# Performance work log

Measured on AMD Instinct MI355X. Metric: run time of the kernel, lower is better.

The kernel has to match this reference:

```python
import jax, jax.numpy as jnp
import numpy as np

D = 1024
H = 16
HD = D // H
FF = 4 * D
EPS = 1e-5


def _layernorm(x, scale, shift):
    # Faithful to the torch module: unbiased std (ddof=1), eps added to std.
    mean = jnp.mean(x, axis=-1, keepdims=True)
    var = jnp.sum((x - mean) ** 2, axis=-1, keepdims=True) / (x.shape[-1] - 1)
    std = jnp.sqrt(var)
    return shift + scale * (x - mean) / (std + EPS)


def _gelu(x):
    c = jnp.sqrt(jnp.asarray(2.0 / jnp.pi, dtype=x.dtype))
    return 0.5 * x * (1.0 + jnp.tanh(c * (x + 0.044715 * x ** 3)))


def setup_inputs() -> dict:
    key = jax.random.key(0)
    ks = jax.random.split(key, 8)
    B, S = 2, 2048
    inv = 1.0 / np.sqrt(D)
    x = jax.random.normal(ks[0], (B, S, D), dtype=jnp.float32)
    scale1 = jnp.ones((D,), jnp.float32)
    shift1 = jnp.zeros((D,), jnp.float32)
    Wqkv = jax.random.normal(ks[1], (3 * D, D), jnp.float32) * inv  # torch layout [out,in]
    Wo_w = jax.random.normal(ks[2], (D, D), jnp.float32) * inv
    Wo_b = jnp.zeros((D,), jnp.float32)
    scale2 = jnp.ones((D,), jnp.float32)
    shift2 = jnp.zeros((D,), jnp.float32)
    W1 = jax.random.normal(ks[3], (FF, D), jnp.float32) * inv
    b1 = jnp.zeros((FF,), jnp.float32)
    W2 = jax.random.normal(ks[4], (D, FF), jnp.float32) * (1.0 / np.sqrt(FF))
    b2 = jnp.zeros((D,), jnp.float32)
    return {"x": x, "scale1": scale1, "shift1": shift1, "Wqkv": Wqkv,
            "Wo_w": Wo_w, "Wo_b": Wo_b, "scale2": scale2, "shift2": shift2,
            "W1": W1, "b1": b1, "W2": W2, "b2": b2}


def reference(x, scale1, shift1, Wqkv, Wo_w, Wo_b, scale2, shift2, W1, b1, W2, b2):
    B, S, _ = x.shape
    # --- pre-norm attention ---
    h = _layernorm(x, scale1, shift1)
    qkv = jnp.einsum('bsd,ed->bse', h, Wqkv)  # [B,S,3D]
    q, k, v = jnp.split(qkv, 3, axis=-1)
    q = q.reshape(B, S, H, HD).transpose(0, 2, 1, 3)  # [B,H,S,HD]
    k = k.reshape(B, S, H, HD).transpose(0, 2, 1, 3)
    v = v.reshape(B, S, H, HD).transpose(0, 2, 1, 3)
    scores = jnp.einsum('bhqd,bhkd->bhqk', q, k) / jnp.sqrt(jnp.asarray(HD, x.dtype))
    causal = jnp.triu(jnp.ones((S, S), dtype=bool), k=1)
    scores = jnp.where(causal, -jnp.inf, scores)
    weights = jax.nn.softmax(scores, axis=-1)
    attn = jnp.einsum('bhqk,bhkd->bhqd', weights, v)
    attn = attn.transpose(0, 2, 1, 3).reshape(B, S, D)
    attn = jnp.einsum('bsd,ed->bse', attn, Wo_w) + Wo_b
    x = x + attn
    # --- pre-norm MLP ---
    h2 = _layernorm(x, scale2, shift2)
    m = _gelu(jnp.einsum('bsd,fd->bsf', h2, W1) + b1)
    m = jnp.einsum('bsf,df->bsd', m, W2) + b2
    return x + m
```

## Files before the change

kernel.cpp:

```cpp
#include <hip/hip_runtime.h>
#include <cstdint>
#include <cstddef>

typedef __bf16 bf16;
typedef __bf16 v8bf __attribute__((ext_vector_type(8)));
typedef __bf16 v4bf __attribute__((ext_vector_type(4)));
typedef float  v4f  __attribute__((ext_vector_type(4)));

#define D_MODEL 1024
#define FF_DIM  4096
#define SEQ     2048
#define NTOK    4096
#define NH      16
#define HDIM    64

#define GLOAD_LDS16(g, l) \
    __builtin_amdgcn_global_load_lds((const __attribute__((address_space(1))) void*)(g), \
                                     (__attribute__((address_space(3))) void*)(l), 16, 0, 0)

__global__ __launch_bounds__(256) void prep_kernel(
    const float* __restrict__ Wqkv, const float* __restrict__ Wo,
    const float* __restrict__ W1, const float* __restrict__ W2,
    bf16* __restrict__ Wqkv_b, bf16* __restrict__ Wo_b,
    bf16* __restrict__ W1_b, bf16* __restrict__ W2_b) {
    int u = blockIdx.x * 256 + threadIdx.x;
    const float* src; bf16* dst; int idx;
    if (u < 786432)       { src = Wqkv; dst = Wqkv_b; idx = u * 4; }
    else if (u < 1048576) { src = Wo;   dst = Wo_b;   idx = (u - 786432) * 4; }
    else if (u < 2097152) { src = W1;   dst = W1_b;   idx = (u - 1048576) * 4; }
    else                  { src = W2;   dst = W2_b;   idx = (u - 2097152) * 4; }
    float4 v = *(const float4*)(src + idx);
    dst[idx + 0] = (bf16)v.x;
    dst[idx + 1] = (bf16)v.y;
    dst[idx + 2] = (bf16)v.z;
    dst[idx + 3] = (bf16)v.w;
}

__global__ __launch_bounds__(256) void layernorm_kernel(
    const float* __restrict__ x, const float* __restrict__ scale,
    const float* __restrict__ shift, bf16* __restrict__ out) {
    int row = blockIdx.x;
    int t = threadIdx.x;
    const float* xr = x + (size_t)row * D_MODEL;
    float4 v = *(const float4*)(xr + t * 4);
    float s  = v.x + v.y + v.z + v.w;
    float sq = v.x * v.x + v.y * v.y + v.z * v.z + v.w * v.w;
    #pragma unroll
    for (int o = 1; o < 64; o <<= 1) {
        s  += __shfl_xor(s, o);
        sq += __shfl_xor(sq, o);
    }
    __shared__ float ws[8];
    int wv = t >> 6;
    if ((t & 63) == 0) { ws[wv * 2] = s; ws[wv * 2 + 1] = sq; }
    __syncthreads();
    s  = ws[0] + ws[2] + ws[4] + ws[6];
    sq = ws[1] + ws[3] + ws[5] + ws[7];
    float mean = s * (1.0f / D_MODEL);
    float var  = (sq - (float)D_MODEL * mean * mean) * (1.0f / (D_MODEL - 1));
    var = fmaxf(var, 0.0f);
    float inv = 1.0f / (sqrtf(var) + 1e-5f);
    #pragma unroll
    for (int j = 0; j < 4; ++j) {
        int c = t * 4 + j;
        float xv = (&v.x)[j];
        out[(size_t)row * D_MODEL + c] = (bf16)(shift[c] + scale[c] * (xv - mean) * inv);
    }
}

__global__ __launch_bounds__(256) void transpose_v(
    const bf16* __restrict__ vb, bf16* __restrict__ vt) {
    int bh = blockIdx.x >> 5;
    int ts = blockIdx.x & 31;
    int t = threadIdx.x;
    __shared__ bf16 T[64][72];
    const bf16* src = vb + ((size_t)bh * SEQ + ts * 64) * HDIM;
    #pragma unroll
    for (int half = 0; half < 2; ++half) {
        int s = (t >> 3) + half * 32;
        int d0 = (t & 7) * 8;
        v8bf vv = *(const v8bf*)(src + (size_t)s * HDIM + d0);
        #pragma unroll
        for (int j = 0; j < 8; ++j) T[d0 + j][s] = vv[j];
    }
    __syncthreads();
    bf16* dst = vt + (size_t)bh * HDIM * SEQ + ts * 64;
    int d = t >> 2;
    #pragma unroll
    for (int cc = 0; cc < 2; ++cc) {
        int c = (t & 3) + cc * 4;
        v8bf o = *(const v8bf*)(&T[d][c * 8]);
        *(v8bf*)(dst + (size_t)d * SEQ + c * 8) = o;
    }
}

template <int EPI>
__global__ __launch_bounds__(256) void gemm_nt(
    const bf16* __restrict__ A, const bf16* __restrict__ Bw,
    const float* __restrict__ bias, const float* __restrict__ resid,
    float* __restrict__ outf, bf16* __restrict__ ob0,
    bf16* __restrict__ ob1, bf16* __restrict__ ob2,
    int M, int N, int K, int klen) {
    __shared__ __align__(16) bf16 As[128 * 64];
    __shared__ __align__(16) bf16 Bs[128 * 64];
    int m0 = blockIdx.y * 128, n0 = blockIdx.x * 128;
    int kstart = blockIdx.z * klen;
    int t = threadIdx.x;
    int lane = t & 63, wave = t >> 6;
    int wm = wave >> 1, wn = wave & 1;
    int quad = lane >> 4, l16 = lane & 15;

    int srow8 = lane >> 3;
    int schunk = (lane & 7) ^ srow8;
    const bf16* agp = A  + (size_t)(m0 + wave * 8 + srow8) * K + kstart + schunk * 8;
    const bf16* bgp = Bw + (size_t)(n0 + wave * 8 + srow8) * K + kstart + schunk * 8;
    size_t row32 = (size_t)32 * K;

    v4f acc[4][4];
    #pragma unroll
    for (int i = 0; i < 4; ++i)
        #pragma unroll
        for (int j = 0; j < 4; ++j)
            acc[i][j] = (v4f){0.f, 0.f, 0.f, 0.f};

    int rsw = l16 & 7;
    for (int kk = 0; kk < klen; kk += 64) {
        __syncthreads();
        #pragma unroll
        for (int ii = 0; ii < 4; ++ii) {
            GLOAD_LDS16(agp + ii * row32 + kk, &As[ii * 2048 + wave * 512]);
            GLOAD_LDS16(bgp + ii * row32 + kk, &Bs[ii * 2048 + wave * 512]);
        }
        __syncthreads();
        #pragma unroll
        for (int h = 0; h < 2; ++h) {
            v8bf af[4], bfr[4];
            #pragma unroll
            for (int i = 0; i < 4; ++i)
                af[i] = *(const v8bf*)(&As[(wm * 64 + i * 16 + l16) * 64 + (((h * 4 + quad) ^ rsw)) * 8]);
            #pragma unroll
            for (int j = 0; j < 4; ++j)
                bfr[j] = *(const v8bf*)(&Bs[(wn * 64 + j * 16 + l16) * 64 + (((h * 4 + quad) ^ rsw)) * 8]);
            #pragma unroll
            for (int i = 0; i < 4; ++i)
                #pragma unroll
                for (int j = 0; j < 4; ++j)
                    acc[i][j] = __builtin_amdgcn_mfma_f32_16x16x32_bf16(af[i], bfr[j], acc[i][j], 0, 0, 0);
        }
    }

    #pragma unroll
    for (int i = 0; i < 4; ++i) {
        #pragma unroll
        for (int j = 0; j < 4; ++j) {
            #pragma unroll
            for (int r = 0; r < 4; ++r) {
                float v = acc[i][j][r];
                int row = m0 + wm * 64 + i * 16 + quad * 4 + r;
                int col = n0 + wn * 64 + j * 16 + l16;
                if (EPI == 0) {
                    int which = col >> 10, rr = col & 1023;
                    int h = rr >> 6, d = rr & 63;
                    int b = row >> 11, sI = row & 2047;
                    size_t dst = (((size_t)(b * NH + h)) * SEQ + sI) * HDIM + d;
                    if (which == 0)      ob0[dst] = (bf16)(v * 0.125f);
                    else if (which == 1) ob1[dst] = (bf16)v;
                    else                 ob2[dst] = (bf16)v;
                } else if (EPI == 1) {
                    size_t o = (size_t)row * N + col;
                    outf[o] = resid[o] + v + bias[col];
                } else if (EPI == 2) {
                    float u = v + bias[col];
                    float y = 1.5957691216057308f * (u + 0.044715f * u * u * u);
                    float g = u * __builtin_amdgcn_rcpf(1.0f + __expf(-y));
                    ob0[(size_t)row * N + col] = (bf16)g;
                } else {
                    ob0[(size_t)blockIdx.z * M * N + (size_t)row * N + col] = (bf16)v;
                }
            }
        }
    }
}

__global__ __launch_bounds__(256) void combine_w2(
    const bf16* __restrict__ part, const float* __restrict__ x1,
    const float* __restrict__ b2, float* __restrict__ out) {
    int i = (blockIdx.x * 256 + threadIdx.x) * 4;
    int col = i & (D_MODEL - 1);
    float4 xv = *(const float4*)(x1 + i);
    float4 bv = *(const float4*)(b2 + col);
    float4 r;
    r.x = xv.x + bv.x; r.y = xv.y + bv.y; r.z = xv.z + bv.z; r.w = xv.w + bv.w;
    #pragma unroll
    for (int z = 0; z < 4; ++z) {
        v4bf p = *(const v4bf*)(part + (size_t)z * NTOK * D_MODEL + i);
        r.x += (float)p[0]; r.y += (float)p[1]; r.z += (float)p[2]; r.w += (float)p[3];
    }
    *(float4*)(out + i) = r;
}

__global__ __launch_bounds__(256) void attn_kernel(
    const bf16* __restrict__ qb, const bf16* __restrict__ kb,
    const bf16* __restrict__ vt, float* __restrict__ pO0,
    float* __restrict__ pO1, float* __restrict__ L0,
    float* __restrict__ L1) {
    int u = (int)gridDim.x - 1 - (int)blockIdx.x;
    int bh = u / 48;
    int r48 = u - bh * 48;
    int qt, st;
    if (r48 < 16) { qt = r48; st = 0; }
    else          { qt = 16 + ((r48 - 16) >> 1); st = (r48 - 16) & 1; }
    int qbase = qt * 64;
    int kv0 = st * 1024;
    int kv1 = min(qbase + 64, kv0 + 1024);
    float* pO = st ? pO1 : pO0;
    float* L  = st ? L1 : L0;

    int t = threadIdx.x;
    int wave = t >> 6, lane = t & 63;
    int quad = lane >> 4, l16 = lane & 15;
    int qwb = qbase + wave * 16;

    const bf16* Qh  = qb + (size_t)bh * SEQ * HDIM;
    const bf16* Kh  = kb + (size_t)bh * SEQ * HDIM;
    const bf16* Vth = vt + (size_t)bh * HDIM * SEQ;

    __shared__ __align__(16) bf16 Ks[64 * 64];
    __shared__ __align__(16) bf16 Vs[64 * 64];
    __shared__ __align__(16) bf16 Ps[4][16 * 80];
    bf16* Pw = &Ps[wave][0];

    int u0 = t, u1 = t + 256;
    int key0 = u0 >> 3, c0 = (u0 & 7) ^ (key0 & 7);
    int key1 = u1 >> 3, c1 = (u1 & 7) ^ (key1 & 7);
    bf16* kdst0 = &Ks[wave * 512];
    bf16* kdst1 = &Ks[2048 + wave * 512];
    bf16* vdst0 = &Vs[wave * 512];
    bf16* vdst1 = &Vs[2048 + wave * 512];
    const bf16* Ksrc0 = Kh + (size_t)key0 * HDIM + c0 * 8;
    const bf16* Ksrc1 = Kh + (size_t)key1 * HDIM + c1 * 8;
    const bf16* Vsrc0 = Vth + (size_t)key0 * SEQ + c0 * 8;
    const bf16* Vsrc1 = Vth + (size_t)key1 * SEQ + c1 * 8;

    v8bf qf0 = *(const v8bf*)(Qh + (size_t)(qwb + l16) * HDIM + quad * 8);
    v8bf qf1 = *(const v8bf*)(Qh + (size_t)(qwb + l16) * HDIM + 32 + quad * 8);

    v4f o[4];
    #pragma unroll
    for (int dc = 0; dc < 4; ++dc) o[dc] = (v4f){0.f, 0.f, 0.f, 0.f};
    float lsum = 0.f;

    for (int kv = kv0; kv < kv1; kv += 64) {
        __syncthreads();
        GLOAD_LDS16(Ksrc0 + (size_t)kv * HDIM, kdst0);
        GLOAD_LDS16(Ksrc1 + (size_t)kv * HDIM, kdst1);
        GLOAD_LDS16(Vsrc0 + kv, vdst0);
        GLOAD_LDS16(Vsrc1 + kv, vdst1);
        __syncthreads();

        bool domask = (kv + 63 > qwb);
        #pragma unroll
        for (int j = 0; j < 4; ++j) {
            int key = j * 16 + l16;
            v8bf ka = *(const v8bf*)(&Ks[(key * 8 + (quad ^ (key & 7))) * 8]);
            v8bf kc = *(const v8bf*)(&Ks[(key * 8 + ((quad + 4) ^ (key & 7))) * 8]);
            v4f s = (v4f){-20.f, -20.f, -20.f, -20.f};
            s = __builtin_amdgcn_mfma_f32_16x16x32_bf16(ka, qf0, s, 0, 0, 0);
            s = __builtin_amdgcn_mfma_f32_16x16x32_bf16(kc, qf1, s, 0, 0, 0);
            int keyb = kv + j * 16 + quad * 4;
            union { bf16 h[4]; uint2 u; } pk;
            #pragma unroll
            for (int r = 0; r < 4; ++r) {
                float pv = __expf(s[r]);
                if (domask) pv = (keyb + r <= qwb + l16) ? pv : 0.f;
                lsum += pv;
                pk.h[r] = (bf16)pv;
            }
            *(uint2*)(&Pw[l16 * 80 + j * 16 + quad * 4]) = pk.u;
        }

        v8bf pf0 = *(const v8bf*)(&Pw[l16 * 80 + quad * 8]);
        v8bf pf1 = *(const v8bf*)(&Pw[l16 * 80 + 32 + quad * 8]);
        #pragma unroll
        for (int dc = 0; dc < 4; ++dc) {
            int dim = dc * 16 + l16;
            v8bf va = *(const v8bf*)(&Vs[(dim * 8 + (quad ^ (dim & 7))) * 8]);
            v8bf vc = *(const v8bf*)(&Vs[(dim * 8 + ((quad + 4) ^ (dim & 7))) * 8]);
            o[dc] = __builtin_amdgcn_mfma_f32_16x16x32_bf16(pf0, va, o[dc], 0, 0, 0);
            o[dc] = __builtin_amdgcn_mfma_f32_16x16x32_bf16(pf1, vc, o[dc], 0, 0, 0);
        }
    }

    lsum += __shfl_xor(lsum, 16);
    lsum += __shfl_xor(lsum, 32);
    if (quad == 0) L[(size_t)bh * SEQ + qwb + l16] = lsum;

    #pragma unroll
    for (int r = 0; r < 4; ++r) {
        int row = qwb + quad * 4 + r;
        #pragma unroll
        for (int dc = 0; dc < 4; ++dc) {
            pO[((size_t)bh * SEQ + row) * HDIM + dc * 16 + l16] = o[dc][r];
        }
    }
}

__global__ __launch_bounds__(256) void attn_finalize(
    const float* __restrict__ pO0, const float* __restrict__ pO1,
    const float* __restrict__ L0, const float* __restrict__ L1,
    bf16* __restrict__ ob) {
    int i = (blockIdx.x * 256 + threadIdx.x) * 4;
    int bh = i >> 17;
    int rem = i & 131071;
    int s = rem >> 6, d0 = rem & 63;
    float l = L0[(size_t)bh * SEQ + s];
    float4 o = *(const float4*)(pO0 + i);
    if ((s >> 6) >= 16) {
        l += L1[(size_t)bh * SEQ + s];
        float4 o1 = *(const float4*)(pO1 + i);
        o.x += o1.x; o.y += o1.y; o.z += o1.z; o.w += o1.w;
    }
    float inv = 1.0f / l;
    int b = bh >> 4, h = bh & 15;
    bf16* dst = ob + ((size_t)(b * SEQ + s)) * D_MODEL + h * HDIM + d0;
    dst[0] = (bf16)(o.x * inv);
    dst[1] = (bf16)(o.y * inv);
    dst[2] = (bf16)(o.z * inv);
    dst[3] = (bf16)(o.w * inv);
}

extern "C" void kernel_launch(void* const* d_in, const int* in_sizes, int n_in,
                              void* d_out, int out_size, void* d_ws, size_t ws_size,
                              hipStream_t stream) {
    const float* x      = (const float*)d_in[0];
    const float* scale1 = (const float*)d_in[1];
    const float* shift1 = (const float*)d_in[2];
    const float* Wqkv   = (const float*)d_in[3];
    const float* Wo_w   = (const float*)d_in[4];
    const float* Wo_b   = (const float*)d_in[5];
    const float* scale2 = (const float*)d_in[6];
    const float* shift2 = (const float*)d_in[7];
    const float* W1     = (const float*)d_in[8];
    const float* b1     = (const float*)d_in[9];
    const float* W2     = (const float*)d_in[10];
    const float* b2     = (const float*)d_in[11];
    float* out = (float*)d_out;

    char* ws = (char*)d_ws;
    size_t off = 0;
    auto alloc = [&](size_t bytes) -> char* {
        char* p = ws + off;
        off += (bytes + 255) & ~(size_t)255;
        return p;
    };
    bf16* Wqkv_b = (bf16*)alloc((size_t)3 * D_MODEL * D_MODEL * 2);
    bf16* Wo_bf  = (bf16*)alloc((size_t)D_MODEL * D_MODEL * 2);
    bf16* W1_b   = (bf16*)alloc((size_t)FF_DIM * D_MODEL * 2);
    bf16* W2_b   = (bf16*)alloc((size_t)D_MODEL * FF_DIM * 2);
    bf16* bufA   = (bf16*)alloc((size_t)NTOK * D_MODEL * 2);
    bf16* qb     = (bf16*)alloc((size_t)NTOK * D_MODEL * 2);
    bf16* kb     = (bf16*)alloc((size_t)NTOK * D_MODEL * 2);
    bf16* vb     = (bf16*)alloc((size_t)NTOK * D_MODEL * 2);
    bf16* vtb    = (bf16*)alloc((size_t)NTOK * D_MODEL * 2);
    float* x1    = (float*)alloc((size_t)NTOK * D_MODEL * 4);
    bf16* mbuf   = (bf16*)alloc((size_t)NTOK * FF_DIM * 2);
    float* pO0 = (float*)mbuf;
    float* L0  = pO0 + (size_t)32 * SEQ * HDIM;
    float* L1  = L0 + (size_t)32 * SEQ;
    float* pO1 = x1;
    bf16* w2part = bufA;
    (void)ws_size; (void)n_in; (void)in_sizes; (void)out_size;

    prep_kernel<<<12288, 256, 0, stream>>>(Wqkv, Wo_w, W1, W2,
                                           Wqkv_b, Wo_bf, W1_b, W2_b);

    layernorm_kernel<<<NTOK, 256, 0, stream>>>(x, scale1, shift1, bufA);

    gemm_nt<0><<<dim3(3072 / 128, NTOK / 128), 256, 0, stream>>>(
        bufA, Wqkv_b, nullptr, nullptr, nullptr, qb, kb, vb, NTOK, 3072, D_MODEL, D_MODEL);

    transpose_v<<<1024, 256, 0, stream>>>(vb, vtb);

    attn_kernel<<<1536, 256, 0, stream>>>(qb, kb, vtb, pO0, pO1, L0, L1);
    attn_finalize<<<32 * SEQ * HDIM / 1024, 256, 0, stream>>>(pO0, pO1, L0, L1, bufA);

    gemm_nt<1><<<dim3(D_MODEL / 128, NTOK / 128), 256, 0, stream>>>(
        bufA, Wo_bf, Wo_b, x, x1, nullptr, nullptr, nullptr, NTOK, D_MODEL, D_MODEL, D_MODEL);

    layernorm_kernel<<<NTOK, 256, 0, stream>>>(x1, scale2, shift2, qb);

    gemm_nt<2><<<dim3(FF_DIM / 128, NTOK / 128), 256, 0, stream>>>(
        qb, W1_b, b1, nullptr, nullptr, mbuf, nullptr, nullptr, NTOK, FF_DIM, D_MODEL, D_MODEL);

    gemm_nt<6><<<dim3(D_MODEL / 128, NTOK / 128, 4), 256, 0, stream>>>(
        mbuf, W2_b, nullptr, nullptr, nullptr, w2part, nullptr, nullptr, NTOK, D_MODEL, FF_DIM, FF_DIM / 4);

    combine_w2<<<NTOK * D_MODEL / 1024, 256, 0, stream>>>(w2part, x1, b2, out);
}
```

Before: 361.4 us.

## Pair causal query tiles per block, skip masked subtiles, fuse attention finalize

Attention now gives each block two query tiles (tile i and tile 31-i) so every block has the same causal workload, and K/V tiles loaded once are shared between the two tiles. Work past the diagonal is skipped at 16/32-key granularity. Normalisation moves into the kernel epilogue, which removes the split-KV partial buffers and the separate finalize launch. Softmax switches to exp2 by folding log2e into the Q scale and the fixed max shift. The grid shrinks to 512 blocks of 256 threads, so occupancy may fall, and each block must keep two sets of accumulators in registers.

```diff
diff --git a/kernel.cpp b/kernel.cpp
--- a/kernel.cpp
+++ b/kernel.cpp
@@ -17,6 +17,9 @@
 #define GLOAD_LDS16(g, l) \
     __builtin_amdgcn_global_load_lds((const __attribute__((address_space(1))) void*)(g), \
                                      (__attribute__((address_space(3))) void*)(l), 16, 0, 0)
+
+#define QSCALE 0.18033688011112042f
+#define SHIFT2 -28.853900817779268f
 
 __global__ __launch_bounds__(256) void prep_kernel(
     const float* __restrict__ Wqkv, const float* __restrict__ Wo,
@@ -163,7 +166,7 @@
                     int h = rr >> 6, d = rr & 63;
                     int b = row >> 11, sI = row & 2047;
                     size_t dst = (((size_t)(b * NH + h)) * SEQ + sI) * HDIM + d;
-                    if (which == 0)      ob0[dst] = (bf16)(v * 0.125f);
+                    if (which == 0)      ob0[dst] = (bf16)(v * QSCALE);
                     else if (which == 1) ob1[dst] = (bf16)v;
                     else                 ob2[dst] = (bf16)v;
                 } else if (EPI == 1) {
@@ -199,27 +202,62 @@
     *(float4*)(out + i) = r;
 }
 
+__device__ __forceinline__ void attn_process_tile(
+    int kv, int qwb, int quad, int l16,
+    const bf16* Ks, const bf16* Vs, bf16* Pw,
+    const v8bf& qf0, const v8bf& qf1, v4f (&o)[4], float& lsum) {
+    #pragma unroll
+    for (int hh = 0; hh < 2; ++hh) {
+        int kb32 = kv + hh * 32;
+        if (kb32 > qwb + 15) break;
+        #pragma unroll
+        for (int j2 = 0; j2 < 2; ++j2) {
+            int j = hh * 2 + j2;
+            int kb16 = kb32 + j2 * 16;
+            union { bf16 h[4]; uint2 u; } pk;
+            if (kb16 > qwb + 15) {
+                pk.u = (uint2){0u, 0u};
+            } else {
+                int key = j * 16 + l16;
+                v8bf ka = *(const v8bf*)(&Ks[(key * 8 + (quad ^ (key & 7))) * 8]);
+                v8bf kc = *(const v8bf*)(&Ks[(key * 8 + ((quad + 4) ^ (key & 7))) * 8]);
+                v4f s = (v4f){SHIFT2, SHIFT2, SHIFT2, SHIFT2};
+                s = __builtin_amdgcn_mfma_f32_16x16x32_bf16(ka, qf0, s, 0, 0, 0);
+                s = __builtin_amdgcn_mfma_f32_16x16x32_bf16(kc, qf1, s, 0, 0, 0);
+                bool dm = (kb16 + 15 > qwb);
+                int keyb = kb16 + quad * 4;
+                #pragma unroll
+                for (int r = 0; r < 4; ++r) {
+                    float pv = __builtin_amdgcn_exp2f(s[r]);
+                    if (dm) pv = (keyb + r <= qwb + l16) ? pv : 0.f;
+                    lsum += pv;
+                    pk.h[r] = (bf16)pv;
+                }
+            }
+            *(uint2*)(&Pw[l16 * 80 + j * 16 + quad * 4]) = pk.u;
+        }
+        v8bf pf = *(const v8bf*)(&Pw[l16 * 80 + hh * 32 + quad * 8]);
+        #pragma unroll
+        for (int dc = 0; dc < 4; ++dc) {
+            int dim = dc * 16 + l16;
+            v8bf vv = *(const v8bf*)(&Vs[(dim * 8 + ((quad + 4 * hh) ^ (dim & 7))) * 8]);
+            o[dc] = __builtin_amdgcn_mfma_f32_16x16x32_bf16(pf, vv, o[dc], 0, 0, 0);
+        }
+    }
+}
+
 __global__ __launch_bounds__(256) void attn_kernel(
     const bf16* __restrict__ qb, const bf16* __restrict__ kb,
-    const bf16* __restrict__ vt, float* __restrict__ pO0,
-    float* __restrict__ pO1, float* __restrict__ L0,
-    float* __restrict__ L1) {
-    int u = (int)gridDim.x - 1 - (int)blockIdx.x;
-    int bh = u / 48;
-    int r48 = u - bh * 48;
-    int qt, st;
-    if (r48 < 16) { qt = r48; st = 0; }
-    else          { qt = 16 + ((r48 - 16) >> 1); st = (r48 - 16) & 1; }
-    int qbase = qt * 64;
-    int kv0 = st * 1024;
-    int kv1 = min(qbase + 64, kv0 + 1024);
-    float* pO = st ? pO1 : pO0;
-    float* L  = st ? L1 : L0;
+    const bf16* __restrict__ vt, bf16* __restrict__ ob) {
+    int bh = blockIdx.x >> 4;
+    int pr = blockIdx.x & 15;
+    int qtA = pr, qtB = 31 - pr;
 
     int t = threadIdx.x;
     int wave = t >> 6, lane = t & 63;
     int quad = lane >> 4, l16 = lane & 15;
-    int qwb = qbase + wave * 16;
+    int qwbA = qtA * 64 + wave * 16;
+    int qwbB = qtB * 64 + wave * 16;
 
     const bf16* Qh  = qb + (size_t)bh * SEQ * HDIM;
     const bf16* Kh  = kb + (size_t)bh * SEQ * HDIM;
@@ -242,91 +280,50 @@
     const bf16* Vsrc0 = Vth + (size_t)key0 * SEQ + c0 * 8;
     const bf16* Vsrc1 = Vth + (size_t)key1 * SEQ + c1 * 8;
 
-    v8bf qf0 = *(const v8bf*)(Qh + (size_t)(qwb + l16) * HDIM + quad * 8);
-    v8bf qf1 = *(const v8bf*)(Qh + (size_t)(qwb + l16) * HDIM + 32 + quad * 8);
-
-    v4f o[4];
-    #pragma unroll
-    for (int dc = 0; dc < 4; ++dc) o[dc] = (v4f){0.f, 0.f, 0.f, 0.f};
-    float lsum = 0.f;
-
-    for (int kv = kv0; kv < kv1; kv += 64) {
+    v8bf qfA0 = *(const v8bf*)(Qh + (size_t)(qwbA + l16) * HDIM + quad * 8);
+    v8bf qfA1 = *(const v8bf*)(Qh + (size_t)(qwbA + l16) * HDIM + 32 + quad * 8);
+    v8bf qfB0 = *(const v8bf*)(Qh + (size_t)(qwbB + l16) * HDIM + quad * 8);
+    v8bf qfB1 = *(const v8bf*)(Qh + (size_t)(qwbB + l16) * HDIM + 32 + quad * 8);
+
+    v4f oA[4], oB[4];
+    #pragma unroll
+    for (int dc = 0; dc < 4; ++dc) {
+        oA[dc] = (v4f){0.f, 0.f, 0.f, 0.f};
+        oB[dc] = (v4f){0.f, 0.f, 0.f, 0.f};
+    }
+    float lA = 0.f, lB = 0.f;
+
+    int kvendA = qtA * 64 + 64;
+    int kvendB = qtB * 64 + 64;
+    for (int kv = 0; kv < kvendB; kv += 64) {
         __syncthreads();
         GLOAD_LDS16(Ksrc0 + (size_t)kv * HDIM, kdst0);
         GLOAD_LDS16(Ksrc1 + (size_t)kv * HDIM, kdst1);
         GLOAD_LDS16(Vsrc0 + kv, vdst0);
         GLOAD_LDS16(Vsrc1 + kv, vdst1);
         __syncthreads();
-
-        bool domask = (kv + 63 > qwb);
-        #pragma unroll
-        for (int j = 0; j < 4; ++j) {
-            int key = j * 16 + l16;
-            v8bf ka = *(const v8bf*)(&Ks[(key * 8 + (quad ^ (key & 7))) * 8]);
-            v8bf kc = *(const v8bf*)(&Ks[(key * 8 + ((quad + 4) ^ (key & 7))) * 8]);
-            v4f s = (v4f){-20.f, -20.f, -20.f, -20.f};
-            s = __builtin_amdgcn_mfma_f32_16x16x32_bf16(ka, qf0, s, 0, 0, 0);
-            s = __builtin_amdgcn_mfma_f32_16x16x32_bf16(kc, qf1, s, 0, 0, 0);
-            int keyb = kv + j * 16 + quad * 4;
-            union { bf16 h[4]; uint2 u; } pk;
-            #pragma unroll
-            for (int r = 0; r < 4; ++r) {
-                float pv = __expf(s[r]);
-                if (domask) pv = (keyb + r <= qwb + l16) ? pv : 0.f;
-                lsum += pv;
-                pk.h[r] = (bf16)pv;
-            }
-            *(uint2*)(&Pw[l16 * 80 + j * 16 + quad * 4]) = pk.u;
-        }
-
-        v8bf pf0 = *(const v8bf*)(&Pw[l16 * 80 + quad * 8]);
-        v8bf pf1 = *(const v8bf*)(&Pw[l16 * 80 + 32 + quad * 8]);
+        if (kv < kvendA)
+            attn_process_tile(kv, qwbA, quad, l16, Ks, Vs, Pw, qfA0, qfA1, oA, lA);
+        attn_process_tile(kv, qwbB, quad, l16, Ks, Vs, Pw, qfB0, qfB1, oB, lB);
+    }
+
+    lA += __shfl_xor(lA, 16); lA += __shfl_xor(lA, 32);
+    lB += __shfl_xor(lB, 16); lB += __shfl_xor(lB, 32);
+
+    int b = bh >> 4, h = bh & 15;
+    #pragma unroll
+    for (int r = 0; r < 4; ++r) {
+        float invA = 1.0f / __shfl(lA, quad * 4 + r);
+        float invB = 1.0f / __shfl(lB, quad * 4 + r);
+        int sA = qwbA + quad * 4 + r;
+        int sB = qwbB + quad * 4 + r;
         #pragma unroll
         for (int dc = 0; dc < 4; ++dc) {
-            int dim = dc * 16 + l16;
-            v8bf va = *(const v8bf*)(&Vs[(dim * 8 + (quad ^ (dim & 7))) * 8]);
-            v8bf vc = *(const v8bf*)(&Vs[(dim * 8 + ((quad + 4) ^ (dim & 7))) * 8]);
-            o[dc] = __builtin_amdgcn_mfma_f32_16x16x32_bf16(pf0, va, o[dc], 0, 0, 0);
-            o[dc] = __builtin_amdgcn_mfma_f32_16x16x32_bf16(pf1, vc, o[dc], 0, 0, 0);
-        }
-    }
-
-    lsum += __shfl_xor(lsum, 16);
-    lsum += __shfl_xor(lsum, 32);
-    if (quad == 0) L[(size_t)bh * SEQ + qwb + l16] = lsum;
-
-    #pragma unroll
-    for (int r = 0; r < 4; ++r) {
-        int row = qwb + quad * 4 + r;
-        #pragma unroll
-        for (int dc = 0; dc < 4; ++dc) {
-            pO[((size_t)bh * SEQ + row) * HDIM + dc * 16 + l16] = o[dc][r];
-        }
-    }
-}
-
-__global__ __launch_bounds__(256) void attn_finalize(
-    const float* __restrict__ pO0, const float* __restrict__ pO1,
-    const float* __restrict__ L0, const float* __restrict__ L1,
-    bf16* __restrict__ ob) {
-    int i = (blockIdx.x * 256 + threadIdx.x) * 4;
-    int bh = i >> 17;
-    int rem = i & 131071;
-    int s = rem >> 6, d0 = rem & 63;
-    float l = L0[(size_t)bh * SEQ + s];
-    float4 o = *(const float4*)(pO0 + i);
-    if ((s >> 6) >= 16) {
-        l += L1[(size_t)bh * SEQ + s];
-        float4 o1 = *(const float4*)(pO1 + i);
-        o.x += o1.x; o.y += o1.y; o.z += o1.z; o.w += o1.w;
-    }
-    float inv = 1.0f / l;
-    int b = bh >> 4, h = bh & 15;
-    bf16* dst = ob + ((size_t)(b * SEQ + s)) * D_MODEL + h * HDIM + d0;
-    dst[0] = (bf16)(o.x * inv);
-    dst[1] = (bf16)(o.y * inv);
-    dst[2] = (bf16)(o.z * inv);
-    dst[3] = (bf16)(o.w * inv);
+            int d = dc * 16 + l16;
+            ob[((size_t)(b * SEQ + sA)) * D_MODEL + h * HDIM + d] = (bf16)(oA[dc][r] * invA);
+            ob[((size_t)(b * SEQ + sB)) * D_MODEL + h * HDIM + d] = (bf16)(oB[dc][r] * invB);
+        }
+    }
 }
 
 extern "C" void kernel_launch(void* const* d_in, const int* in_sizes, int n_in,
@@ -364,10 +361,6 @@
     bf16* vtb    = (bf16*)alloc((size_t)NTOK * D_MODEL * 2);
     float* x1    = (float*)alloc((size_t)NTOK * D_MODEL * 4);
     bf16* mbuf   = (bf16*)alloc((size_t)NTOK * FF_DIM * 2);
-    float* pO0 = (float*)mbuf;
-    float* L0  = pO0 + (size_t)32 * SEQ * HDIM;
-    float* L1  = L0 + (size_t)32 * SEQ;
-    float* pO1 = x1;
     bf16* w2part = bufA;
     (void)ws_size; (void)n_in; (void)in_sizes; (void)out_size;
 
@@ -381,8 +374,7 @@
 
     transpose_v<<<1024, 256, 0, stream>>>(vb, vtb);
 
-    attn_kernel<<<1536, 256, 0, stream>>>(qb, kb, vtb, pO0, pO1, L0, L1);
-    attn_finalize<<<32 * SEQ * HDIM / 1024, 256, 0, stream>>>(pO0, pO1, L0, L1, bufA);
+    attn_kernel<<<512, 256, 0, stream>>>(qb, kb, vtb, bufA);
 
     gemm_nt<1><<<dim3(D_MODEL / 128, NTOK / 128), 256, 0, stream>>>(
         bufA, Wo_bf, Wo_b, x, x1, nullptr, nullptr, nullptr, NTOK, D_MODEL, D_MODEL, D_MODEL);
```

Result: no change. 360.8 us (-0.2%).
